# Kernel optimization log

Measured on AMD Instinct MI355X. Metric: run time of the kernel, lower is better.

The kernel has to match this reference:

```python
import jax, jax.numpy as jnp
import numpy as np

D_MODEL = 256
NUM_HEADS = 8
D_HEAD = D_MODEL // NUM_HEADS


def setup_inputs() -> dict:
    key = jax.random.key(0)
    k1, k2, k3, k4, k5, k6 = jax.random.split(key, 6)
    B, L, C, H, W = 2, 2048, D_MODEL, 4, 4
    query = jax.random.normal(k1, (B, L, C, H, W), dtype=jnp.float32)
    key_t = jax.random.normal(k2, (B, L, C, H, W), dtype=jnp.float32)
    value = jax.random.normal(k3, (B, L, C, H, W), dtype=jnp.float32)
    # 1x1 conv weights (out_channels, in_channels), no bias
    s = 1.0 / np.sqrt(C)
    Wq = jax.random.uniform(k4, (C, C), jnp.float32, -s, s)
    Wk = jax.random.uniform(k5, (C, C), jnp.float32, -s, s)
    Wv = jax.random.uniform(k6, (C, C), jnp.float32, -s, s)
    return {"query": query, "key": key_t, "value": value, "Wq": Wq, "Wk": Wk, "Wv": Wv}


def _split_heads(x, B, L, H, W):
    # (B, L, C, H, W) -> (num_heads*B, L, d_head, H, W), head-major like torch permute(2,0,1,3,4,5)
    x = x.reshape(B, L, NUM_HEADS, D_HEAD, H, W)
    x = jnp.transpose(x, (2, 0, 1, 3, 4, 5))  # (nh, B, L, d_head, H, W)
    return x.reshape(NUM_HEADS * B, L, D_HEAD, H, W)


def reference(query, key, value, Wq, Wk, Wv):
    B, L, C, H, W = value.shape
    # 1x1 conv == channel matmul: (B,L,C,H,W) x (O,C) -> (B,L,O,H,W)
    q = jnp.einsum('blchw,oc->blohw', query, Wq)
    k = jnp.einsum('blchw,oc->blohw', key, Wk)
    v = jnp.einsum('blchw,oc->blohw', value, Wv)
    q = _split_heads(q, B, L, H, W)
    k = _split_heads(k, B, L, H, W)
    v = _split_heads(v, B, L, H, W)
    scale = 1.0 / np.sqrt(D_HEAD).astype(np.float32)
    score = jnp.einsum('bidhw,bjdhw->bij', q, k) * scale  # (nh*B, L, L)
    attn = jax.nn.softmax(score, axis=-1)
    context = jnp.einsum('bij,bjdhw->bidhw', attn, v)  # (nh*B, L, d_head, H, W)
    context = context.reshape(NUM_HEADS, B, L, D_HEAD, H, W)
    context = jnp.transpose(context, (1, 2, 0, 3, 4, 5)).reshape(B, L, C, H, W)
    return context, attn
```

## Files before the change

### kernel.cpp

```cpp
#include <hip/hip_runtime.h>


typedef short s16x8 __attribute__((ext_vector_type(8)));
typedef float f32x4 __attribute__((ext_vector_type(4)));

__device__ __forceinline__ unsigned short f2bf(float f) {
  union { float f; unsigned int u; } v; v.f = f;
  return (unsigned short)((v.u + 0x7FFFu + ((v.u >> 16) & 1u)) >> 16);
}
__device__ __forceinline__ float bf2f(unsigned short h) {
  union { unsigned int u; float f; } v; v.u = ((unsigned int)h) << 16;
  return v.f;
}

__device__ __forceinline__ void async_copy16(const unsigned short* g, unsigned short* l) {
  __builtin_amdgcn_global_load_lds((const __attribute__((address_space(1))) void*)g,
                                   (__attribute__((address_space(3))) void*)l, 16, 0, 0);
}

__global__ void __launch_bounds__(256) prep_all_kernel(const float* __restrict__ qs,
                                                       const float* __restrict__ ks,
                                                       const float* __restrict__ vs,
                                                       unsigned short* __restrict__ Xq,
                                                       unsigned short* __restrict__ Xk,
                                                       unsigned short* __restrict__ X2) {
  __shared__ float ld[256 * 17];
  const int bl = blockIdx.x;
  const int z = blockIdx.y;
  const int t = threadIdx.x;
  const float* s = (z == 0 ? qs : (z == 1 ? ks : vs)) + (size_t)bl * 4096;
#pragma unroll
  for (int i = 0; i < 4; ++i) {
    int flat = i * 1024 + t * 4;
    float4 v = *(const float4*)(s + flat);
    int c = flat >> 4, hw = flat & 15;
    float* p = &ld[c * 17 + hw];
    p[0] = v.x; p[1] = v.y; p[2] = v.z; p[3] = v.w;
  }
  __syncthreads();
  if (z < 2) {
    unsigned short* d = (z == 0 ? Xq : Xk) + (size_t)bl * 4096;
#pragma unroll
    for (int hw = 0; hw < 16; ++hw)
      d[hw * 256 + t] = f2bf(ld[t * 17 + hw]);
  } else {
    const int b = bl >> 11, l = bl & 2047;
#pragma unroll
    for (int hw = 0; hw < 16; ++hw)
      X2[((size_t)(b * 16 + hw) * 2048 + l) * 256 + t] = f2bf(ld[t * 17 + hw]);
  }
}

__global__ void __launch_bounds__(256) prep_x_kernel(const float* __restrict__ src,
                                                     unsigned short* __restrict__ dst) {
  __shared__ float ld[256 * 17];
  const int bl = blockIdx.x;
  const int t = threadIdx.x;
  const float* s = src + (size_t)bl * 4096;
#pragma unroll
  for (int i = 0; i < 4; ++i) {
    int flat = i * 1024 + t * 4;
    float4 v = *(const float4*)(s + flat);
    int c = flat >> 4, hw = flat & 15;
    float* p = &ld[c * 17 + hw];
    p[0] = v.x; p[1] = v.y; p[2] = v.z; p[3] = v.w;
  }
  __syncthreads();
  unsigned short* d = dst + (size_t)bl * 4096;
#pragma unroll
  for (int hw = 0; hw < 16; ++hw)
    d[hw * 256 + t] = f2bf(ld[t * 17 + hw]);
}

__global__ void __launch_bounds__(256) prep_w_kernel(const float* __restrict__ a,
                                                     const float* __restrict__ b,
                                                     const float* __restrict__ c,
                                                     unsigned short* __restrict__ dst) {
  int i = blockIdx.x * 256 + threadIdx.x;
  const float* s = (i < 65536) ? a : ((i < 131072) ? b : c);
  dst[i] = f2bf(s[i & 65535]);
}

__device__ __forceinline__ void gemm_core_async(const unsigned short* __restrict__ Ag, int ldA,
                                                const unsigned short* __restrict__ Bg, int ldB,
                                                int K, unsigned short* As, unsigned short* Bs,
                                                f32x4 acc[4][4]) {
  const int tid = threadIdx.x;
  const int lane = tid & 63;
  const int w = tid >> 6;
  const int wr = (w >> 1) * 64, wc = (w & 1) * 64;
  const int r = lane >> 2, kk = (lane & 3) * 8;
  for (int k0 = 0; k0 < K; k0 += 32) {
#pragma unroll
    for (int i = 0; i < 2; ++i) {
      const int row0 = w * 32 + i * 16;
      async_copy16(Ag + (size_t)(row0 + r) * ldA + k0 + kk, As + row0 * 32);
      async_copy16(Bg + (size_t)(row0 + r) * ldB + k0 + kk, Bs + row0 * 32);
    }
    __syncthreads();
    s16x8 af[4], bfv[4];
#pragma unroll
    for (int m = 0; m < 4; ++m)
      af[m] = *(const s16x8*)(As + (wr + m * 16 + (lane & 15)) * 32 + (lane >> 4) * 8);
#pragma unroll
    for (int n = 0; n < 4; ++n)
      bfv[n] = *(const s16x8*)(Bs + (wc + n * 16 + (lane & 15)) * 32 + (lane >> 4) * 8);
#pragma unroll
    for (int m = 0; m < 4; ++m)
#pragma unroll
      for (int n = 0; n < 4; ++n)
        acc[m][n] = __builtin_amdgcn_mfma_f32_16x16x32_bf16(af[m], bfv[n], acc[m][n], 0, 0, 0);
    __syncthreads();
  }
}

#define ACC_INIT(acc)                         \
  {                                           \
    const f32x4 z_ = {0.f, 0.f, 0.f, 0.f};    \
    _Pragma("unroll")                         \
    for (int m_ = 0; m_ < 4; ++m_)            \
      _Pragma("unroll")                       \
      for (int n_ = 0; n_ < 4; ++n_) acc[m_][n_] = z_; \
  }

__global__ void __launch_bounds__(256) gemm_proj_qk_kernel(const unsigned short* __restrict__ Xq,
                                                           const unsigned short* __restrict__ Xk,
                                                           const unsigned short* __restrict__ Wbf,
                                                           unsigned short* __restrict__ q_s,
                                                           unsigned short* __restrict__ k_s) {
  __shared__ unsigned short As[4096], Bs[4096];
  f32x4 acc[4][4];
  ACC_INIT(acc);
  const int z = blockIdx.z;
  const unsigned short* X = z ? Xk : Xq;
  const unsigned short* W = Wbf + z * 65536;
  unsigned short* out = z ? k_s : q_s;
  gemm_core_async(X + (size_t)blockIdx.x * 128 * 256, 256,
                  W + (size_t)blockIdx.y * 128 * 256, 256, 256, As, Bs, acc);
  const int tid = threadIdx.x, lane = tid & 63, w = tid >> 6;
  const int wr = (w >> 1) * 64, wc = (w & 1) * 64;
  const int R0 = blockIdx.x * 128 + wr + ((lane >> 4) << 2);
  const int C0 = blockIdx.y * 128 + wc + (lane & 15);
#pragma unroll
  for (int m = 0; m < 4; ++m)
#pragma unroll
    for (int n = 0; n < 4; ++n)
#pragma unroll
      for (int r = 0; r < 4; ++r) {
        int R = R0 + m * 16 + r;
        int o = C0 + n * 16;
        int bl = R >> 4, hw = R & 15;
        int b = bl >> 11, l = bl & 2047;
        int head = o >> 5, d = o & 31;
        out[((size_t)(head * 2 + b) * 2048 + l) * 512 + d * 16 + hw] = f2bf(acc[m][n][r]);
      }
}

__global__ void __launch_bounds__(256) gemm_proj_kernel(const unsigned short* __restrict__ X,
                                                        const unsigned short* __restrict__ W,
                                                        unsigned short* __restrict__ out) {
  __shared__ unsigned short As[4096], Bs[4096];
  f32x4 acc[4][4];
  ACC_INIT(acc);
  gemm_core_async(X + (size_t)blockIdx.x * 128 * 256, 256,
                  W + (size_t)blockIdx.y * 128 * 256, 256, 256, As, Bs, acc);
  const int tid = threadIdx.x, lane = tid & 63, w = tid >> 6;
  const int wr = (w >> 1) * 64, wc = (w & 1) * 64;
  const int R0 = blockIdx.x * 128 + wr + ((lane >> 4) << 2);
  const int C0 = blockIdx.y * 128 + wc + (lane & 15);
#pragma unroll
  for (int m = 0; m < 4; ++m)
#pragma unroll
    for (int n = 0; n < 4; ++n)
#pragma unroll
      for (int r = 0; r < 4; ++r) {
        int R = R0 + m * 16 + r;
        int o = C0 + n * 16;
        int bl = R >> 4, hw = R & 15;
        int b = bl >> 11, l = bl & 2047;
        int head = o >> 5, d = o & 31;
        out[((size_t)(head * 2 + b) * 2048 + l) * 512 + d * 16 + hw] = f2bf(acc[m][n][r]);
      }
}

__global__ void __launch_bounds__(256) gemm_proj_vt_kernel(const unsigned short* __restrict__ W,
                                                           const unsigned short* __restrict__ X2,
                                                           unsigned short* __restrict__ vt) {
  __shared__ unsigned short As[4096], Bs[4096];
  f32x4 acc[4][4];
  ACC_INIT(acc);
  gemm_core_async(W + (size_t)blockIdx.x * 128 * 256, 256,
                  X2 + (size_t)blockIdx.y * 128 * 256, 256, 256, As, Bs, acc);
  const int tid = threadIdx.x, lane = tid & 63, w = tid >> 6;
  const int wr = (w >> 1) * 64, wc = (w & 1) * 64;
  const int R0 = blockIdx.x * 128 + wr + ((lane >> 4) << 2);
  const int C0 = blockIdx.y * 128 + wc + (lane & 15);
#pragma unroll
  for (int m = 0; m < 4; ++m)
#pragma unroll
    for (int n = 0; n < 4; ++n)
#pragma unroll
      for (int r = 0; r < 4; ++r) {
        int o = R0 + m * 16 + r;
        int p = C0 + n * 16;
        int head = o >> 5, d = o & 31;
        int b = p >> 15, hw = (p >> 11) & 15, l = p & 2047;
        vt[((size_t)((head * 2 + b) * 512) + d * 16 + hw) * 2048 + l] = f2bf(acc[m][n][r]);
      }
}

template <int FUSED>
__global__ void __launch_bounds__(256) gemm_score_kernel(const unsigned short* __restrict__ q,
                                                         const unsigned short* __restrict__ k,
                                                         float* __restrict__ attn,
                                                         unsigned short* __restrict__ pbf,
                                                         float* __restrict__ partial) {
  __shared__ unsigned short As[4096], Bs[4096];
  f32x4 acc[4][4];
  ACC_INIT(acc);
  const int bh = blockIdx.z;
  gemm_core_async(q + ((size_t)bh * 2048 + blockIdx.x * 128) * 512, 512,
                  k + ((size_t)bh * 2048 + blockIdx.y * 128) * 512, 512, 512, As, Bs, acc);
  const int tid = threadIdx.x, lane = tid & 63, w = tid >> 6;
  const int wr = (w >> 1) * 64, wc = (w & 1) * 64;
  const float scale = 0.17677669529663687f;
  const int R0 = blockIdx.x * 128 + wr + ((lane >> 4) << 2);
  const int C0 = blockIdx.y * 128 + wc + (lane & 15);
  if (!FUSED) {
    float* O = attn + (size_t)bh * 4194304;
#pragma unroll
    for (int m = 0; m < 4; ++m)
#pragma unroll
      for (int n = 0; n < 4; ++n)
#pragma unroll
        for (int r = 0; r < 4; ++r)
          O[(size_t)(R0 + m * 16 + r) * 2048 + (C0 + n * 16)] = acc[m][n][r] * scale;
  } else {
#pragma unroll
    for (int m = 0; m < 4; ++m)
#pragma unroll
      for (int n = 0; n < 4; ++n)
#pragma unroll
        for (int r = 0; r < 4; ++r)
          acc[m][n][r] = __expf(acc[m][n][r] * scale);
    unsigned short* P = pbf + (size_t)bh * 4194304;
#pragma unroll
    for (int m = 0; m < 4; ++m)
#pragma unroll
      for (int n = 0; n < 4; ++n)
#pragma unroll
        for (int r = 0; r < 4; ++r)
          P[(size_t)(R0 + m * 16 + r) * 2048 + (C0 + n * 16)] = f2bf(acc[m][n][r]);
    const int chunk = blockIdx.y * 2 + (w & 1);
#pragma unroll
    for (int m = 0; m < 4; ++m)
#pragma unroll
      for (int r = 0; r < 4; ++r) {
        float s = (acc[m][0][r] + acc[m][1][r]) + (acc[m][2][r] + acc[m][3][r]);
        s += __shfl_xor(s, 1); s += __shfl_xor(s, 2);
        s += __shfl_xor(s, 4); s += __shfl_xor(s, 8);
        if ((lane & 15) == 0) {
          int rloc = wr + ((lane >> 4) << 2) + m * 16 + r;
          partial[((size_t)bh * 2048 + blockIdx.x * 128 + rloc) * 32 + chunk] = s;
        }
      }
  }
}

__global__ void __launch_bounds__(256) inv_kernel(const float* __restrict__ partial,
                                                  float* __restrict__ inv_buf) {
  const int t = threadIdx.x;
  const int row = blockIdx.x * 64 + (t >> 2);
  const int q4 = t & 3;
  const float4* p = (const float4*)(partial + (size_t)row * 32 + q4 * 8);
  float4 a = p[0], b = p[1];
  float s = ((a.x + a.y) + (a.z + a.w)) + ((b.x + b.y) + (b.z + b.w));
  s += __shfl_xor(s, 1); s += __shfl_xor(s, 2);
  if (q4 == 0) inv_buf[row] = 1.0f / s;
}

__device__ __forceinline__ void ctx_epilogue(f32x4 acc[4][4], float* __restrict__ outc,
                                             const float* __restrict__ inv_buf,
                                             int bh, int bx, int by) {
  const int tid = threadIdx.x, lane = tid & 63, w = tid >> 6;
  const int wr = (w >> 1) * 64, wc = (w & 1) * 64;
  const int b = bh & 1, head = bh >> 1;
  const int R0 = bx * 128 + wr + ((lane >> 4) << 2);
  const int C0 = by * 128 + wc + (lane & 15);
#pragma unroll
  for (int m = 0; m < 4; ++m)
#pragma unroll
    for (int r2 = 0; r2 < 4; ++r2) {
      int R = R0 + m * 16 + r2;
      float sc = inv_buf ? inv_buf[(size_t)bh * 2048 + R] : 1.0f;
#pragma unroll
      for (int n = 0; n < 4; ++n) {
        int dd = C0 + n * 16;
        int d = dd >> 4, hw = dd & 15;
        outc[((size_t)(b * 2048 + R) * 256 + head * 32 + d) * 16 + hw] = acc[m][n][r2] * sc;
      }
    }
}

__global__ void __launch_bounds__(256) gemm_ctx_fused_kernel(const unsigned short* __restrict__ pbf,
                                                             const unsigned short* __restrict__ vt,
                                                             const float* __restrict__ inv_buf,
                                                             float* __restrict__ attn,
                                                             float* __restrict__ outc) {
  __shared__ unsigned short As[4096], Bs[4096];
  f32x4 acc[4][4];
  ACC_INIT(acc);
  const int tid = threadIdx.x, lane = tid & 63, w = tid >> 6;
  const int wr = (w >> 1) * 64, wc = (w & 1) * 64;
  const int bh = blockIdx.z;
  const unsigned short* Ag = pbf + (size_t)bh * 4194304 + (size_t)blockIdx.x * 128 * 2048;
  const unsigned short* Bg = vt + (size_t)bh * 1048576 + (size_t)blockIdx.y * 128 * 2048;
  const int r = lane >> 2, kk = (lane & 3) * 8;
  const bool emit = (blockIdx.y == 0);
  const int erow = tid >> 1, ecol = (tid & 1) * 16;
  float einv = 0.f;
  float* eattn = nullptr;
  if (emit) {
    einv = inv_buf[(size_t)bh * 2048 + blockIdx.x * 128 + erow];
    eattn = attn + (size_t)bh * 4194304 + (size_t)(blockIdx.x * 128 + erow) * 2048 + ecol;
  }
  for (int k0 = 0; k0 < 2048; k0 += 32) {
#pragma unroll
    for (int i = 0; i < 2; ++i) {
      const int row0 = w * 32 + i * 16;
      async_copy16(Ag + (size_t)(row0 + r) * 2048 + k0 + kk, As + row0 * 32);
      async_copy16(Bg + (size_t)(row0 + r) * 2048 + k0 + kk, Bs + row0 * 32);
    }
    __syncthreads();
    if (emit) {
      s16x8 h0 = *(const s16x8*)(As + erow * 32 + ecol);
      s16x8 h1 = *(const s16x8*)(As + erow * 32 + ecol + 8);
      float o[16];
#pragma unroll
      for (int i = 0; i < 8; ++i) o[i] = bf2f((unsigned short)h0[i]) * einv;
#pragma unroll
      for (int i = 0; i < 8; ++i) o[8 + i] = bf2f((unsigned short)h1[i]) * einv;
      float* ep = eattn + k0;
      *(float4*)(ep)      = *(float4*)&o[0];
      *(float4*)(ep + 4)  = *(float4*)&o[4];
      *(float4*)(ep + 8)  = *(float4*)&o[8];
      *(float4*)(ep + 12) = *(float4*)&o[12];
    }
    s16x8 af[4], bfv[4];
#pragma unroll
    for (int m = 0; m < 4; ++m)
      af[m] = *(const s16x8*)(As + (wr + m * 16 + (lane & 15)) * 32 + (lane >> 4) * 8);
#pragma unroll
    for (int n = 0; n < 4; ++n)
      bfv[n] = *(const s16x8*)(Bs + (wc + n * 16 + (lane & 15)) * 32 + (lane >> 4) * 8);
#pragma unroll
    for (int m = 0; m < 4; ++m)
#pragma unroll
      for (int n = 0; n < 4; ++n)
        acc[m][n] = __builtin_amdgcn_mfma_f32_16x16x32_bf16(af[m], bfv[n], acc[m][n], 0, 0, 0);
    __syncthreads();
  }
  ctx_epilogue(acc, outc, inv_buf, bh, blockIdx.x, blockIdx.y);
}

__global__ void __launch_bounds__(256) softmax_kernel(float* __restrict__ attn) {
  __shared__ float red[4];
  float* p = attn + (size_t)blockIdx.x * 2048;
  const int t = threadIdx.x;
  float4 v0 = *(const float4*)(p + t * 8);
  float4 v1 = *(const float4*)(p + t * 8 + 4);
  float mx = fmaxf(fmaxf(fmaxf(v0.x, v0.y), fmaxf(v0.z, v0.w)),
                   fmaxf(fmaxf(v1.x, v1.y), fmaxf(v1.z, v1.w)));
#pragma unroll
  for (int off = 32; off; off >>= 1) mx = fmaxf(mx, __shfl_xor(mx, off));
  if ((t & 63) == 0) red[t >> 6] = mx;
  __syncthreads();
  mx = fmaxf(fmaxf(red[0], red[1]), fmaxf(red[2], red[3]));
  __syncthreads();
  float e[8];
  e[0] = __expf(v0.x - mx); e[1] = __expf(v0.y - mx);
  e[2] = __expf(v0.z - mx); e[3] = __expf(v0.w - mx);
  e[4] = __expf(v1.x - mx); e[5] = __expf(v1.y - mx);
  e[6] = __expf(v1.z - mx); e[7] = __expf(v1.w - mx);
  float s = ((e[0] + e[1]) + (e[2] + e[3])) + ((e[4] + e[5]) + (e[6] + e[7]));
#pragma unroll
  for (int off = 32; off; off >>= 1) s += __shfl_xor(s, off);
  if ((t & 63) == 0) red[t >> 6] = s;
  __syncthreads();
  s = red[0] + red[1] + red[2] + red[3];
  const float inv = 1.0f / s;
  float4 o0 = {e[0] * inv, e[1] * inv, e[2] * inv, e[3] * inv};
  float4 o1 = {e[4] * inv, e[5] * inv, e[6] * inv, e[7] * inv};
  *(float4*)(p + t * 8) = o0;
  *(float4*)(p + t * 8 + 4) = o1;
}

__global__ void __launch_bounds__(256) transpose_v_kernel(const unsigned short* __restrict__ vs,
                                                          unsigned short* __restrict__ vt) {
  __shared__ unsigned short tile[64][65];
  const int bh = blockIdx.z;
  const int j0 = blockIdx.x * 64, d0 = blockIdx.y * 64;
  const unsigned short* src = vs + (size_t)bh * 2048 * 512;
  unsigned short* dst = vt + (size_t)bh * 512 * 2048;
  const int t = threadIdx.x;
#pragma unroll
  for (int i = 0; i < 16; ++i) {
    int e = t * 16 + i;
    int r = e >> 6, c = e & 63;
    tile[r][c] = src[(size_t)(j0 + r) * 512 + d0 + c];
  }
  __syncthreads();
#pragma unroll
  for (int i = 0; i < 16; ++i) {
    int e = t * 16 + i;
    int r = e >> 6, c = e & 63;
    dst[(size_t)(d0 + r) * 2048 + j0 + c] = tile[c][r];
  }
}

__global__ void __launch_bounds__(256) gemm_ctx_f32_kernel(const float* __restrict__ attn,
                                                           const unsigned short* __restrict__ vt,
                                                           float* __restrict__ outc) {
  __shared__ unsigned short As[4096], Bs[4096];
  f32x4 acc[4][4];
  ACC_INIT(acc);
  const int tid = threadIdx.x, lane = tid & 63, w = tid >> 6;
  const int wr = (w >> 1) * 64, wc = (w & 1) * 64;
  const int bh = blockIdx.z;
  const float* Ag = attn + (size_t)bh * 4194304 + (size_t)blockIdx.x * 128 * 2048;
  const unsigned short* Bg = vt + (size_t)bh * 1048576 + (size_t)blockIdx.y * 128 * 2048;
  const int r = lane >> 2, kk = (lane & 3) * 8;
  const int arow = tid >> 1, acol = (tid & 1) * 16;
  for (int k0 = 0; k0 < 2048; k0 += 32) {
#pragma unroll
    for (int i = 0; i < 2; ++i) {
      const int row0 = w * 32 + i * 16;
      async_copy16(Bg + (size_t)(row0 + r) * 2048 + k0 + kk, Bs + row0 * 32);
    }
    {
      const float* sp = Ag + (size_t)arow * 2048 + k0 + acol;
      float4 f0 = *(const float4*)(sp);
      float4 f1 = *(const float4*)(sp + 4);
      float4 f2 = *(const float4*)(sp + 8);
      float4 f3 = *(const float4*)(sp + 12);
      s16x8 h0, h1;
      h0[0] = (short)f2bf(f0.x); h0[1] = (short)f2bf(f0.y);
      h0[2] = (short)f2bf(f0.z); h0[3] = (short)f2bf(f0.w);
      h0[4] = (short)f2bf(f1.x); h0[5] = (short)f2bf(f1.y);
      h0[6] = (short)f2bf(f1.z); h0[7] = (short)f2bf(f1.w);
      h1[0] = (short)f2bf(f2.x); h1[1] = (short)f2bf(f2.y);
      h1[2] = (short)f2bf(f2.z); h1[3] = (short)f2bf(f2.w);
      h1[4] = (short)f2bf(f3.x); h1[5] = (short)f2bf(f3.y);
      h1[6] = (short)f2bf(f3.z); h1[7] = (short)f2bf(f3.w);
      *(s16x8*)(As + arow * 32 + acol) = h0;
      *(s16x8*)(As + arow * 32 + acol + 8) = h1;
    }
    __syncthreads();
    s16x8 af[4], bfv[4];
#pragma unroll
    for (int m = 0; m < 4; ++m)
      af[m] = *(const s16x8*)(As + (wr + m * 16 + (lane & 15)) * 32 + (lane >> 4) * 8);
#pragma unroll
    for (int n = 0; n < 4; ++n)
      bfv[n] = *(const s16x8*)(Bs + (wc + n * 16 + (lane & 15)) * 32 + (lane >> 4) * 8);
#pragma unroll
    for (int m = 0; m < 4; ++m)
#pragma unroll
      for (int n = 0; n < 4; ++n)
        acc[m][n] = __builtin_amdgcn_mfma_f32_16x16x32_bf16(af[m], bfv[n], acc[m][n], 0, 0, 0);
    __syncthreads();
  }
  ctx_epilogue(acc, outc, nullptr, bh, blockIdx.x, blockIdx.y);
}

extern "C" void kernel_launch(void* const* d_in, const int* in_sizes, int n_in,
                              void* d_out, int out_size, void* d_ws, size_t ws_size,
                              hipStream_t stream) {
  const float* query = (const float*)d_in[0];
  const float* key   = (const float*)d_in[1];
  const float* value = (const float*)d_in[2];
  const float* Wq    = (const float*)d_in[3];
  const float* Wk    = (const float*)d_in[4];
  const float* Wv    = (const float*)d_in[5];

  float* out_ctx  = (float*)d_out;
  float* out_attn = (float*)d_out + 16777216;

  unsigned short* X2   = (unsigned short*)d_ws;
  unsigned short* q_s  = X2 + 16777216;
  unsigned short* k_s  = q_s + 16777216;
  unsigned short* v_t  = k_s + 16777216;
  unsigned short* Wbf  = v_t + 16777216;
  unsigned short* P_bf = Wbf + 196608;
  float* partial = (float*)(P_bf + 67108864);
  float* inv_buf = partial + 1048576;

  unsigned short* Xq = P_bf;
  unsigned short* Xk = P_bf + 16777216;

  const bool fused = ws_size >= (size_t)273154048;

  prep_w_kernel<<<768, 256, 0, stream>>>(Wq, Wk, Wv, Wbf);

  if (fused) {
    prep_all_kernel<<<dim3(4096, 3), 256, 0, stream>>>(query, key, value, Xq, Xk, X2);
    gemm_proj_qk_kernel<<<dim3(512, 2, 2), 256, 0, stream>>>(Xq, Xk, Wbf, q_s, k_s);
    gemm_proj_vt_kernel<<<dim3(2, 512), 256, 0, stream>>>(Wbf + 131072, X2, v_t);
    gemm_score_kernel<1><<<dim3(16, 16, 16), 256, 0, stream>>>(q_s, k_s, nullptr, P_bf, partial);
    inv_kernel<<<512, 256, 0, stream>>>(partial, inv_buf);
    gemm_ctx_fused_kernel<<<dim3(16, 4, 16), 256, 0, stream>>>(P_bf, v_t, inv_buf, out_attn, out_ctx);
  } else {
    prep_x_kernel<<<4096, 256, 0, stream>>>(query, X2);
    gemm_proj_kernel<<<dim3(512, 2), 256, 0, stream>>>(X2, Wbf, q_s);
    prep_x_kernel<<<4096, 256, 0, stream>>>(key, X2);
    gemm_proj_kernel<<<dim3(512, 2), 256, 0, stream>>>(X2, Wbf + 65536, k_s);
    prep_x_kernel<<<4096, 256, 0, stream>>>(value, X2);
    gemm_proj_kernel<<<dim3(512, 2), 256, 0, stream>>>(X2, Wbf + 131072, v_t);
    gemm_score_kernel<0><<<dim3(16, 16, 16), 256, 0, stream>>>(q_s, k_s, out_attn, nullptr, nullptr);
    softmax_kernel<<<32768, 256, 0, stream>>>(out_attn);
    transpose_v_kernel<<<dim3(32, 8, 16), 256, 0, stream>>>(v_t, X2);
    gemm_ctx_f32_kernel<<<dim3(16, 4, 16), 256, 0, stream>>>(out_attn, X2, out_ctx);
  }
}
```

Measured before the change: 504.9 us.

## Use 256x256 double-buffered swizzled GEMM tiles and a separate attn normalize pass

Score and context GEMMs move from 128x128 single-buffered tiles to 256x256 tiles with 512 threads. Loads go through double-buffered async global-to-LDS copies with an XOR-swizzled LDS layout and raised wave priority around the MFMA blocks. Writing the normalized attn output moves out of the context GEMM into a standalone row-normalize kernel, which also absorbs the inverse-sum kernel. The aim is more operand reuse and overlap of loads with compute, at the cost of fewer blocks, higher register pressure and an extra read of the bf16 P matrix.

```diff
diff --git a/kernel.cpp b/kernel.cpp
--- a/kernel.cpp
+++ b/kernel.cpp
@@ -16,6 +16,155 @@
 __device__ __forceinline__ void async_copy16(const unsigned short* g, unsigned short* l) {
   __builtin_amdgcn_global_load_lds((const __attribute__((address_space(1))) void*)g,
                                    (__attribute__((address_space(3))) void*)l, 16, 0, 0);
+}
+
+
+template <int LD>
+__device__ __forceinline__ void stage256(const unsigned short* __restrict__ Xg,
+                                         unsigned short* __restrict__ lds_base,
+                                         int kt) {
+  const int tid = threadIdx.x;
+  const int wid = tid >> 6, lane = tid & 63;
+  const int prow = lane >> 2, pgran = lane & 3;
+  const int lgran = pgran ^ ((prow >> 1) & 3);
+  const int row0 = wid * 32;
+#pragma unroll
+  for (int i = 0; i < 2; ++i) {
+    const int rb = row0 + i * 16;
+    async_copy16(Xg + (size_t)(rb + prow) * LD + kt * 32 + lgran * 8,
+                 lds_base + rb * 32);
+  }
+}
+
+__device__ __forceinline__ void compute256(const unsigned short* __restrict__ As_,
+                                           const unsigned short* __restrict__ Bs_,
+                                           f32x4 acc[8][4]) {
+  const int tid = threadIdx.x, lane = tid & 63, wid = tid >> 6;
+  const int wm = wid >> 2, wn = wid & 3;
+  const int rl = lane & 15;
+  const int xg = (lane >> 4) ^ ((rl >> 1) & 3);
+  const unsigned short* Aw = As_ + (size_t)(wm * 128 + rl) * 32 + xg * 8;
+  const unsigned short* Bw = Bs_ + (size_t)(wn * 64 + rl) * 32 + xg * 8;
+  s16x8 b[4], a[4];
+#pragma unroll
+  for (int n = 0; n < 4; ++n) b[n] = *(const s16x8*)(Bw + n * 16 * 32);
+#pragma unroll
+  for (int m = 0; m < 4; ++m) a[m] = *(const s16x8*)(Aw + m * 16 * 32);
+  __builtin_amdgcn_s_setprio(1);
+#pragma unroll
+  for (int m = 0; m < 4; ++m)
+#pragma unroll
+    for (int n = 0; n < 4; ++n)
+      acc[m][n] = __builtin_amdgcn_mfma_f32_16x16x32_bf16(a[m], b[n], acc[m][n], 0, 0, 0);
+  __builtin_amdgcn_s_setprio(0);
+#pragma unroll
+  for (int m = 0; m < 4; ++m) a[m] = *(const s16x8*)(Aw + (64 + m * 16) * 32);
+  __builtin_amdgcn_s_setprio(1);
+#pragma unroll
+  for (int m = 0; m < 4; ++m)
+#pragma unroll
+    for (int n = 0; n < 4; ++n)
+      acc[4 + m][n] = __builtin_amdgcn_mfma_f32_16x16x32_bf16(a[m], b[n], acc[4 + m][n], 0, 0, 0);
+  __builtin_amdgcn_s_setprio(0);
+}
+
+template <int LD, int NT>
+__device__ __forceinline__ void gemm256_loop(const unsigned short* __restrict__ Ag,
+                                             const unsigned short* __restrict__ Bg,
+                                             unsigned short (*As)[8192],
+                                             unsigned short (*Bs)[8192],
+                                             f32x4 acc[8][4]) {
+  stage256<LD>(Ag, As[0], 0); stage256<LD>(Bg, Bs[0], 0);
+  stage256<LD>(Ag, As[1], 1); stage256<LD>(Bg, Bs[1], 1);
+  for (int kt = 0; kt < NT; ++kt) {
+    if (kt < NT - 1) asm volatile("s_waitcnt vmcnt(4)" ::: "memory");
+    else             asm volatile("s_waitcnt vmcnt(0)" ::: "memory");
+    __builtin_amdgcn_s_barrier();
+    compute256(As[kt & 1], Bs[kt & 1], acc);
+    __builtin_amdgcn_s_barrier();
+    if (kt + 2 < NT) {
+      stage256<LD>(Ag, As[kt & 1], kt + 2);
+      stage256<LD>(Bg, Bs[kt & 1], kt + 2);
+    }
+  }
+}
+
+#define ACC_INIT8(acc)                        \
+  {                                           \
+    const f32x4 z_ = {0.f, 0.f, 0.f, 0.f};    \
+    _Pragma("unroll")                         \
+    for (int m_ = 0; m_ < 8; ++m_)            \
+      _Pragma("unroll")                       \
+      for (int n_ = 0; n_ < 4; ++n_) acc[m_][n_] = z_; \
+  }
+
+__global__ void __launch_bounds__(512, 2)
+gemm_score256_kernel(const unsigned short* __restrict__ q, const unsigned short* __restrict__ k,
+                     unsigned short* __restrict__ pbf, float* __restrict__ partial) {
+  __shared__ unsigned short As[2][8192], Bs[2][8192];
+  f32x4 acc[8][4];
+  ACC_INIT8(acc);
+  const int bh = blockIdx.z;
+  const unsigned short* Ag = q + ((size_t)bh * 2048 + blockIdx.x * 256) * 512;
+  const unsigned short* Bg = k + ((size_t)bh * 2048 + blockIdx.y * 256) * 512;
+  gemm256_loop<512, 16>(Ag, Bg, As, Bs, acc);
+  const int tid = threadIdx.x, lane = tid & 63, wid = tid >> 6;
+  const int wm = wid >> 2, wn = wid & 3;
+  const float scale = 0.17677669529663687f;
+  const int R0 = blockIdx.x * 256 + wm * 128 + ((lane >> 4) << 2);
+  const int C0 = blockIdx.y * 256 + wn * 64 + (lane & 15);
+  unsigned short* P = pbf + (size_t)bh * 4194304;
+#pragma unroll
+  for (int m = 0; m < 8; ++m)
+#pragma unroll
+    for (int n = 0; n < 4; ++n)
+#pragma unroll
+      for (int r = 0; r < 4; ++r) {
+        float e = __expf(acc[m][n][r] * scale);
+        acc[m][n][r] = e;
+        P[(size_t)(R0 + m * 16 + r) * 2048 + (C0 + n * 16)] = f2bf(e);
+      }
+  const int chunk = blockIdx.y * 4 + wn;
+#pragma unroll
+  for (int m = 0; m < 8; ++m)
+#pragma unroll
+    for (int r = 0; r < 4; ++r) {
+      float s = (acc[m][0][r] + acc[m][1][r]) + (acc[m][2][r] + acc[m][3][r]);
+      s += __shfl_xor(s, 1); s += __shfl_xor(s, 2);
+      s += __shfl_xor(s, 4); s += __shfl_xor(s, 8);
+      if ((lane & 15) == 0)
+        partial[((size_t)bh * 2048 + R0 + m * 16 + r) * 32 + chunk] = s;
+    }
+}
+
+__global__ void __launch_bounds__(512, 2)
+gemm_ctx256_kernel(const unsigned short* __restrict__ pbf, const unsigned short* __restrict__ vt,
+                   const float* __restrict__ inv_buf, float* __restrict__ outc) {
+  __shared__ unsigned short As[2][8192], Bs[2][8192];
+  f32x4 acc[8][4];
+  ACC_INIT8(acc);
+  const int bh = blockIdx.z;
+  const unsigned short* Ag = pbf + (size_t)bh * 4194304 + (size_t)blockIdx.x * 256 * 2048;
+  const unsigned short* Bg = vt + (size_t)bh * 1048576 + (size_t)blockIdx.y * 256 * 2048;
+  gemm256_loop<2048, 64>(Ag, Bg, As, Bs, acc);
+  const int tid = threadIdx.x, lane = tid & 63, wid = tid >> 6;
+  const int wm = wid >> 2, wn = wid & 3;
+  const int b = bh & 1, head = bh >> 1;
+  const int R0 = blockIdx.x * 256 + wm * 128 + ((lane >> 4) << 2);
+  const int C0 = blockIdx.y * 256 + wn * 64 + (lane & 15);
+#pragma unroll
+  for (int m = 0; m < 8; ++m)
+#pragma unroll
+    for (int r = 0; r < 4; ++r) {
+      const int R = R0 + m * 16 + r;
+      const float sc = inv_buf[(size_t)bh * 2048 + R];
+#pragma unroll
+      for (int n = 0; n < 4; ++n) {
+        int dd = C0 + n * 16;
+        outc[((size_t)(b * 2048 + R) * 256 + head * 32 + (dd >> 4)) * 16 + (dd & 15)] =
+            acc[m][n][r] * sc;
+      }
+    }
 }
 
 __global__ void __launch_bounds__(256) prep_all_kernel(const float* __restrict__ qs,
@@ -209,12 +358,34 @@
       }
 }
 
-template <int FUSED>
-__global__ void __launch_bounds__(256) gemm_score_kernel(const unsigned short* __restrict__ q,
-                                                         const unsigned short* __restrict__ k,
-                                                         float* __restrict__ attn,
-                                                         unsigned short* __restrict__ pbf,
-                                                         float* __restrict__ partial) {
+__global__ void __launch_bounds__(256) norm_kernel(const unsigned short* __restrict__ pbf,
+                                                   const float* __restrict__ partial,
+                                                   float* __restrict__ attn,
+                                                   float* __restrict__ inv_buf) {
+  __shared__ float sh;
+  const int row = blockIdx.x;
+  const int t = threadIdx.x;
+  if (t < 32) {
+    float v = partial[(size_t)row * 32 + t];
+    v += __shfl_xor(v, 1); v += __shfl_xor(v, 2);
+    v += __shfl_xor(v, 4); v += __shfl_xor(v, 8); v += __shfl_xor(v, 16);
+    if (t == 0) sh = v;
+  }
+  __syncthreads();
+  const float inv = 1.0f / sh;
+  if (t == 0) inv_buf[row] = inv;
+  s16x8 h = *(const s16x8*)(pbf + (size_t)row * 2048 + t * 8);
+  float o[8];
+#pragma unroll
+  for (int i = 0; i < 8; ++i) o[i] = bf2f((unsigned short)h[i]) * inv;
+  float* p = attn + (size_t)row * 2048 + t * 8;
+  *(float4*)(p)     = *(float4*)&o[0];
+  *(float4*)(p + 4) = *(float4*)&o[4];
+}
+
+__global__ void __launch_bounds__(256) gemm_score_f32_kernel(const unsigned short* __restrict__ q,
+                                                             const unsigned short* __restrict__ k,
+                                                             float* __restrict__ attn) {
   __shared__ unsigned short As[4096], Bs[4096];
   f32x4 acc[4][4];
   ACC_INIT(acc);
@@ -223,144 +394,17 @@
                   k + ((size_t)bh * 2048 + blockIdx.y * 128) * 512, 512, 512, As, Bs, acc);
   const int tid = threadIdx.x, lane = tid & 63, w = tid >> 6;
   const int wr = (w >> 1) * 64, wc = (w & 1) * 64;
+  float* O = attn + (size_t)bh * 4194304;
   const float scale = 0.17677669529663687f;
   const int R0 = blockIdx.x * 128 + wr + ((lane >> 4) << 2);
   const int C0 = blockIdx.y * 128 + wc + (lane & 15);
-  if (!FUSED) {
-    float* O = attn + (size_t)bh * 4194304;
-#pragma unroll
-    for (int m = 0; m < 4; ++m)
-#pragma unroll
-      for (int n = 0; n < 4; ++n)
-#pragma unroll
-        for (int r = 0; r < 4; ++r)
-          O[(size_t)(R0 + m * 16 + r) * 2048 + (C0 + n * 16)] = acc[m][n][r] * scale;
-  } else {
-#pragma unroll
-    for (int m = 0; m < 4; ++m)
-#pragma unroll
-      for (int n = 0; n < 4; ++n)
-#pragma unroll
-        for (int r = 0; r < 4; ++r)
-          acc[m][n][r] = __expf(acc[m][n][r] * scale);
-    unsigned short* P = pbf + (size_t)bh * 4194304;
-#pragma unroll
-    for (int m = 0; m < 4; ++m)
-#pragma unroll
-      for (int n = 0; n < 4; ++n)
-#pragma unroll
-        for (int r = 0; r < 4; ++r)
-          P[(size_t)(R0 + m * 16 + r) * 2048 + (C0 + n * 16)] = f2bf(acc[m][n][r]);
-    const int chunk = blockIdx.y * 2 + (w & 1);
-#pragma unroll
-    for (int m = 0; m < 4; ++m)
-#pragma unroll
-      for (int r = 0; r < 4; ++r) {
-        float s = (acc[m][0][r] + acc[m][1][r]) + (acc[m][2][r] + acc[m][3][r]);
-        s += __shfl_xor(s, 1); s += __shfl_xor(s, 2);
-        s += __shfl_xor(s, 4); s += __shfl_xor(s, 8);
-        if ((lane & 15) == 0) {
-          int rloc = wr + ((lane >> 4) << 2) + m * 16 + r;
-          partial[((size_t)bh * 2048 + blockIdx.x * 128 + rloc) * 32 + chunk] = s;
-        }
-      }
-  }
-}
-
-__global__ void __launch_bounds__(256) inv_kernel(const float* __restrict__ partial,
-                                                  float* __restrict__ inv_buf) {
-  const int t = threadIdx.x;
-  const int row = blockIdx.x * 64 + (t >> 2);
-  const int q4 = t & 3;
-  const float4* p = (const float4*)(partial + (size_t)row * 32 + q4 * 8);
-  float4 a = p[0], b = p[1];
-  float s = ((a.x + a.y) + (a.z + a.w)) + ((b.x + b.y) + (b.z + b.w));
-  s += __shfl_xor(s, 1); s += __shfl_xor(s, 2);
-  if (q4 == 0) inv_buf[row] = 1.0f / s;
-}
-
-__device__ __forceinline__ void ctx_epilogue(f32x4 acc[4][4], float* __restrict__ outc,
-                                             const float* __restrict__ inv_buf,
-                                             int bh, int bx, int by) {
-  const int tid = threadIdx.x, lane = tid & 63, w = tid >> 6;
-  const int wr = (w >> 1) * 64, wc = (w & 1) * 64;
-  const int b = bh & 1, head = bh >> 1;
-  const int R0 = bx * 128 + wr + ((lane >> 4) << 2);
-  const int C0 = by * 128 + wc + (lane & 15);
-#pragma unroll
-  for (int m = 0; m < 4; ++m)
-#pragma unroll
-    for (int r2 = 0; r2 < 4; ++r2) {
-      int R = R0 + m * 16 + r2;
-      float sc = inv_buf ? inv_buf[(size_t)bh * 2048 + R] : 1.0f;
-#pragma unroll
-      for (int n = 0; n < 4; ++n) {
-        int dd = C0 + n * 16;
-        int d = dd >> 4, hw = dd & 15;
-        outc[((size_t)(b * 2048 + R) * 256 + head * 32 + d) * 16 + hw] = acc[m][n][r2] * sc;
-      }
-    }
-}
-
-__global__ void __launch_bounds__(256) gemm_ctx_fused_kernel(const unsigned short* __restrict__ pbf,
-                                                             const unsigned short* __restrict__ vt,
-                                                             const float* __restrict__ inv_buf,
-                                                             float* __restrict__ attn,
-                                                             float* __restrict__ outc) {
-  __shared__ unsigned short As[4096], Bs[4096];
-  f32x4 acc[4][4];
-  ACC_INIT(acc);
-  const int tid = threadIdx.x, lane = tid & 63, w = tid >> 6;
-  const int wr = (w >> 1) * 64, wc = (w & 1) * 64;
-  const int bh = blockIdx.z;
-  const unsigned short* Ag = pbf + (size_t)bh * 4194304 + (size_t)blockIdx.x * 128 * 2048;
-  const unsigned short* Bg = vt + (size_t)bh * 1048576 + (size_t)blockIdx.y * 128 * 2048;
-  const int r = lane >> 2, kk = (lane & 3) * 8;
-  const bool emit = (blockIdx.y == 0);
-  const int erow = tid >> 1, ecol = (tid & 1) * 16;
-  float einv = 0.f;
-  float* eattn = nullptr;
-  if (emit) {
-    einv = inv_buf[(size_t)bh * 2048 + blockIdx.x * 128 + erow];
-    eattn = attn + (size_t)bh * 4194304 + (size_t)(blockIdx.x * 128 + erow) * 2048 + ecol;
-  }
-  for (int k0 = 0; k0 < 2048; k0 += 32) {
-#pragma unroll
-    for (int i = 0; i < 2; ++i) {
-      const int row0 = w * 32 + i * 16;
-      async_copy16(Ag + (size_t)(row0 + r) * 2048 + k0 + kk, As + row0 * 32);
-      async_copy16(Bg + (size_t)(row0 + r) * 2048 + k0 + kk, Bs + row0 * 32);
-    }
-    __syncthreads();
-    if (emit) {
-      s16x8 h0 = *(const s16x8*)(As + erow * 32 + ecol);
-      s16x8 h1 = *(const s16x8*)(As + erow * 32 + ecol + 8);
-      float o[16];
-#pragma unroll
-      for (int i = 0; i < 8; ++i) o[i] = bf2f((unsigned short)h0[i]) * einv;
-#pragma unroll
-      for (int i = 0; i < 8; ++i) o[8 + i] = bf2f((unsigned short)h1[i]) * einv;
-      float* ep = eattn + k0;
-      *(float4*)(ep)      = *(float4*)&o[0];
-      *(float4*)(ep + 4)  = *(float4*)&o[4];
-      *(float4*)(ep + 8)  = *(float4*)&o[8];
-      *(float4*)(ep + 12) = *(float4*)&o[12];
-    }
-    s16x8 af[4], bfv[4];
-#pragma unroll
-    for (int m = 0; m < 4; ++m)
-      af[m] = *(const s16x8*)(As + (wr + m * 16 + (lane & 15)) * 32 + (lane >> 4) * 8);
-#pragma unroll
-    for (int n = 0; n < 4; ++n)
-      bfv[n] = *(const s16x8*)(Bs + (wc + n * 16 + (lane & 15)) * 32 + (lane >> 4) * 8);
-#pragma unroll
-    for (int m = 0; m < 4; ++m)
-#pragma unroll
-      for (int n = 0; n < 4; ++n)
-        acc[m][n] = __builtin_amdgcn_mfma_f32_16x16x32_bf16(af[m], bfv[n], acc[m][n], 0, 0, 0);
-    __syncthreads();
-  }
-  ctx_epilogue(acc, outc, inv_buf, bh, blockIdx.x, blockIdx.y);
+#pragma unroll
+  for (int m = 0; m < 4; ++m)
+#pragma unroll
+    for (int n = 0; n < 4; ++n)
+#pragma unroll
+      for (int r = 0; r < 4; ++r)
+        O[(size_t)(R0 + m * 16 + r) * 2048 + (C0 + n * 16)] = acc[m][n][r] * scale;
 }
 
 __global__ void __launch_bounds__(256) softmax_kernel(float* __restrict__ attn) {
@@ -470,7 +514,20 @@
         acc[m][n] = __builtin_amdgcn_mfma_f32_16x16x32_bf16(af[m], bfv[n], acc[m][n], 0, 0, 0);
     __syncthreads();
   }
-  ctx_epilogue(acc, outc, nullptr, bh, blockIdx.x, blockIdx.y);
+  const int b = bh & 1, head = bh >> 1;
+  const int R0 = blockIdx.x * 128 + wr + ((lane >> 4) << 2);
+  const int C0 = blockIdx.y * 128 + wc + (lane & 15);
+#pragma unroll
+  for (int m = 0; m < 4; ++m)
+#pragma unroll
+    for (int n = 0; n < 4; ++n)
+#pragma unroll
+      for (int r2 = 0; r2 < 4; ++r2) {
+        int R = R0 + m * 16 + r2;
+        int dd = C0 + n * 16;
+        outc[((size_t)(b * 2048 + R) * 256 + head * 32 + (dd >> 4)) * 16 + (dd & 15)] =
+            acc[m][n][r2];
+      }
 }
 
 extern "C" void kernel_launch(void* const* d_in, const int* in_sizes, int n_in,
@@ -506,9 +563,9 @@
     prep_all_kernel<<<dim3(4096, 3), 256, 0, stream>>>(query, key, value, Xq, Xk, X2);
     gemm_proj_qk_kernel<<<dim3(512, 2, 2), 256, 0, stream>>>(Xq, Xk, Wbf, q_s, k_s);
     gemm_proj_vt_kernel<<<dim3(2, 512), 256, 0, stream>>>(Wbf + 131072, X2, v_t);
-    gemm_score_kernel<1><<<dim3(16, 16, 16), 256, 0, stream>>>(q_s, k_s, nullptr, P_bf, partial);
-    inv_kernel<<<512, 256, 0, stream>>>(partial, inv_buf);
-    gemm_ctx_fused_kernel<<<dim3(16, 4, 16), 256, 0, stream>>>(P_bf, v_t, inv_buf, out_attn, out_ctx);
+    gemm_score256_kernel<<<dim3(8, 8, 16), 512, 0, stream>>>(q_s, k_s, P_bf, partial);
+    norm_kernel<<<32768, 256, 0, stream>>>(P_bf, partial, out_attn, inv_buf);
+    gemm_ctx256_kernel<<<dim3(8, 2, 16), 512, 0, stream>>>(P_bf, v_t, inv_buf, out_ctx);
   } else {
     prep_x_kernel<<<4096, 256, 0, stream>>>(query, X2);
     gemm_proj_kernel<<<dim3(512, 2), 256, 0, stream>>>(X2, Wbf, q_s);
@@ -516,7 +573,7 @@
     gemm_proj_kernel<<<dim3(512, 2), 256, 0, stream>>>(X2, Wbf + 65536, k_s);
     prep_x_kernel<<<4096, 256, 0, stream>>>(value, X2);
     gemm_proj_kernel<<<dim3(512, 2), 256, 0, stream>>>(X2, Wbf + 131072, v_t);
-    gemm_score_kernel<0><<<dim3(16, 16, 16), 256, 0, stream>>>(q_s, k_s, out_attn, nullptr, nullptr);
+    gemm_score_f32_kernel<<<dim3(16, 16, 16), 256, 0, stream>>>(q_s, k_s, out_attn);
     softmax_kernel<<<32768, 256, 0, stream>>>(out_attn);
     transpose_v_kernel<<<dim3(32, 8, 16), 256, 0, stream>>>(v_t, X2);
     gemm_ctx_f32_kernel<<<dim3(16, 4, 16), 256, 0, stream>>>(out_attn, X2, out_ctx);
```

After: 416.2 us, median of 2. 1.21x faster.
